# Performance work log

Hardware: AMD Instinct MI355X
Metric: run time of the kernel (lower is better)

Reference implementation:

```python
import jax, jax.numpy as jnp
import numpy as np

DIM = 1024
N_HEADS = 16
HEAD_DIM = DIM // N_HEADS  # 64
THETA = 10000.0
B, S = 4, 1024


def _rope_full_dim(x):
    """RoPE applied over the FULL last dim (head_dim == model dim), matching the
    original module which builds RotaryEmbeddings(head_dim=args.dim) and applies
    it to [B, S, dim] before splitting into heads. Positions start at 0."""
    Bx, Sx, D = x.shape
    freq = 1.0 / (THETA ** (jnp.arange(0, D, 2, dtype=jnp.float32) / D))  # [D/2]
    ang = jnp.arange(Sx, dtype=jnp.float32)[:, None] * freq[None, :]      # [S, D/2]
    cos, sin = jnp.cos(ang), jnp.sin(ang)
    xp = x.astype(jnp.float32).reshape(Bx, Sx, D // 2, 2)
    x0, x1 = xp[..., 0], xp[..., 1]
    rot = jnp.stack([x0 * cos - x1 * sin, x0 * sin + x1 * cos], axis=-1)
    return rot.reshape(Bx, Sx, D).astype(x.dtype)


def setup_inputs() -> dict:
    key = jax.random.key(0)
    ks = jax.random.split(key, 5)
    scale = 1.0 / np.sqrt(DIM)
    x = jax.random.normal(ks[0], (B, S, DIM), dtype=jnp.float32)
    Wq = jax.random.normal(ks[1], (DIM, DIM), dtype=jnp.float32) * scale
    Wk = jax.random.normal(ks[2], (DIM, DIM), dtype=jnp.float32) * scale
    Wv = jax.random.normal(ks[3], (DIM, DIM), dtype=jnp.float32) * scale
    Wo = jax.random.normal(ks[4], (DIM, DIM), dtype=jnp.float32) * scale
    bo = jnp.zeros((DIM,), dtype=jnp.float32)
    return {"x": x, "Wq": Wq, "Wk": Wk, "Wv": Wv, "Wo": Wo, "bo": bo, "start_pos": 0}


def reference(x, Wq, Wk, Wv, Wo, bo, start_pos):
    # start_pos == 0: the zero-initialized KV cache write+read is an identity
    # (keys == xk, values == xv over [:, :S]); n_rep == 1 so repeat_kv is a no-op.
    # NOTE: the original applies NO causal mask.
    Bx, Sx, _ = x.shape
    xq = _rope_full_dim(x @ Wq.T)  # [B, S, DIM] (weights stored torch-style [out,in])
    xk = _rope_full_dim(x @ Wk.T)
    xv = x @ Wv.T
    q = xq.reshape(Bx, Sx, N_HEADS, HEAD_DIM).transpose(0, 2, 1, 3)  # [B,H,S,D]
    k = xk.reshape(Bx, Sx, N_HEADS, HEAD_DIM).transpose(0, 2, 1, 3)
    v = xv.reshape(Bx, Sx, N_HEADS, HEAD_DIM).transpose(0, 2, 1, 3)
    scores = jnp.einsum("bhqd,bhkd->bhqk", q, k) / np.float32(np.sqrt(HEAD_DIM))
    attn = jax.nn.softmax(scores.astype(jnp.float32), axis=-1).astype(q.dtype)
    out = jnp.einsum("bhqk,bhkd->bhqd", attn, v)          # [B,H,S,D]
    out = out.transpose(0, 2, 1, 3).reshape(Bx, Sx, DIM)  # [B,S,DIM]
    return out @ Wo.T + bo
```

## Files before the change

### kernel.cpp

```cpp
#include <hip/hip_runtime.h>
#include <cstdint>
#include <cstddef>

typedef _Float16 f16;
typedef __attribute__((ext_vector_type(8))) _Float16 h8v;
typedef __attribute__((ext_vector_type(4))) _Float16 h4v;
typedef __attribute__((ext_vector_type(4))) float f4v;

#define DIM 1024
#define SEQ 1024
#define NH 16
#define HD 64

__device__ __forceinline__ void gld16(const void* g, void* l) {
  __builtin_amdgcn_global_load_lds(
      (const __attribute__((address_space(1))) void*)g,
      (__attribute__((address_space(3))) void*)l, 16, 0, 0);
}

__device__ __forceinline__ f4v mfma16(h8v a, h8v b, f4v c) {
  return __builtin_amdgcn_mfma_f32_16x16x32_f16(a, b, c, 0, 0, 0);
}
__device__ __forceinline__ f4v mfma16k16(h4v a, h4v b, f4v c) {
  return __builtin_amdgcn_mfma_f32_16x16x16f16(a, b, c, 0, 0, 0);
}

__device__ __forceinline__ void cvt_store4(f16* dst, float4 v) {
  *(h4v*)dst = (h4v){(f16)v.x, (f16)v.y, (f16)v.z, (f16)v.w};
}

__global__ __launch_bounds__(256) void convert_kernel(
    const float* __restrict__ x,  const float* __restrict__ Wq,
    const float* __restrict__ Wk, const float* __restrict__ Wv,
    const float* __restrict__ Wo,
    f16* __restrict__ xh, f16* __restrict__ wqkv, f16* __restrict__ woh)
{
  int i = blockIdx.x * 256 + threadIdx.x;
  cvt_store4(xh + 4 * (size_t)i, ((const float4*)x)[i]);
  if (i < DIM * DIM / 4) {
    cvt_store4(wqkv + 4 * (size_t)i,               ((const float4*)Wq)[i]);
    cvt_store4(wqkv + DIM * DIM + 4 * (size_t)i,   ((const float4*)Wk)[i]);
    cvt_store4(wqkv + 2 * DIM * DIM + 4 * (size_t)i, ((const float4*)Wv)[i]);
    cvt_store4(woh + 4 * (size_t)i,                ((const float4*)Wo)[i]);
  }
}

__global__ __launch_bounds__(256) void qkv_gemm(
    const f16* __restrict__ A, const f16* __restrict__ W,
    f16* __restrict__ Qh, f16* __restrict__ Kh, f16* __restrict__ Vt)
{
  __shared__ f16 lA[128 * 32];
  __shared__ f16 lB[128 * 32];
  const int m0 = blockIdx.x * 128;
  const int n0 = blockIdx.y * 128;
  const int tid = threadIdx.x;
  const int w = tid >> 6, lane = tid & 63, quad = lane >> 4, l16 = lane & 15;
  const int wm = (w >> 1) * 64, wn = (w & 1) * 64;

  const int c0 = tid, c1 = 256 + tid;
  const int r0 = c0 >> 2, kc0 = (c0 & 3) ^ ((r0 >> 1) & 3);
  const int r1 = c1 >> 2, kc1 = (c1 & 3) ^ ((r1 >> 1) & 3);
  const f16* gA0 = A + (size_t)(m0 + r0) * DIM + kc0 * 8;
  const f16* gA1 = A + (size_t)(m0 + r1) * DIM + kc1 * 8;
  const f16* gB0 = W + (size_t)(n0 + r0) * DIM + kc0 * 8;
  const f16* gB1 = W + (size_t)(n0 + r1) * DIM + kc1 * 8;
  f16* lA0 = &lA[(c0 & ~63) * 8];
  f16* lA1 = &lA[(c1 & ~63) * 8];
  f16* lB0 = &lB[(c0 & ~63) * 8];
  f16* lB1 = &lB[(c1 & ~63) * 8];

  int pA[4], pB[4];
#pragma unroll
  for (int t = 0; t < 4; ++t) {
    int r = wm + t * 16 + l16;
    pA[t] = r * 4 + (quad ^ ((r >> 1) & 3));
    int rn = wn + t * 16 + l16;
    pB[t] = rn * 4 + (quad ^ ((rn >> 1) & 3));
  }

  f4v acc[4][4] = {};
  for (int kt = 0; kt < DIM / 32; ++kt) {
    const int ko = kt * 32;
    gld16(gA0 + ko, lA0);
    gld16(gA1 + ko, lA1);
    gld16(gB0 + ko, lB0);
    gld16(gB1 + ko, lB1);
    __syncthreads();
    h8v af[4], bf[4];
#pragma unroll
    for (int t = 0; t < 4; ++t) af[t] = *(const h8v*)&lA[pA[t] * 8];
#pragma unroll
    for (int t = 0; t < 4; ++t) bf[t] = *(const h8v*)&lB[pB[t] * 8];
#pragma unroll
    for (int i = 0; i < 4; ++i)
#pragma unroll
      for (int j = 0; j < 4; ++j)
        acc[i][j] = mfma16(af[i], bf[j], acc[i][j]);
    __syncthreads();
  }

  if (n0 < 2 * DIM) {
    f16* dst = (n0 < DIM) ? Qh : Kh;
    const float osc = (n0 < DIM) ? 0.18033688f : 1.0f;
#pragma unroll
    for (int i = 0; i < 4; ++i) {
      const int mb = m0 + wm + i * 16 + quad * 4;
#pragma unroll
      for (int j = 0; j < 4; ++j) {
        const int n = n0 + wn + j * 16 + l16;
        const int d = n & (DIM - 1);
        const float fr = exp2f(-0.025952563f * (float)(d >> 1));
        const float sgn = (d & 1) ? 1.0f : -1.0f;
        const int hh = d >> 6, dd = d & 63;
#pragma unroll
        for (int r = 0; r < 4; ++r) {
          const int m = mb + r;
          const int s = m & (SEQ - 1), b = m >> 10;
          const float v = acc[i][j][r];
          const float pt = __shfl_xor(v, 1, 64);
          float sn, cs;
          __sincosf((float)s * fr, &sn, &cs);
          dst[((size_t)(b * NH + hh) * SEQ + s) * HD + dd] =
              (f16)((v * cs + sgn * pt * sn) * osc);
        }
      }
    }
  } else {
#pragma unroll
    for (int i = 0; i < 4; ++i) {
      const int mb = m0 + wm + i * 16 + quad * 4;
      const int s = mb & (SEQ - 1), b = mb >> 10;
#pragma unroll
      for (int j = 0; j < 4; ++j) {
        const int d = (n0 - 2 * DIM) + wn + j * 16 + l16;
        const int hh = d >> 6, dd = d & 63;
        h4v vv = {(f16)acc[i][j][0], (f16)acc[i][j][1],
                  (f16)acc[i][j][2], (f16)acc[i][j][3]};
        *(h4v*)&Vt[((size_t)(b * NH + hh) * HD + dd) * SEQ + s] = vv;
      }
    }
  }
}

__global__ __launch_bounds__(256) void attn_kernel(
    const f16* __restrict__ Q, const f16* __restrict__ K,
    const f16* __restrict__ V, f16* __restrict__ O)
{
  __shared__ f16 LK[2][4096];
  __shared__ f16 LV[2][4096];
  const int tid = threadIdx.x;
  const int w = tid >> 6, lane = tid & 63, quad = lane >> 4, l16 = lane & 15;
  const int bid = blockIdx.x;
  const int qt = bid >> 6, bh = bid & 63;
  const f16* Qb = Q + (size_t)bh * SEQ * HD;
  const f16* Kg = K + (size_t)bh * SEQ * HD;
  const f16* Vg = V + (size_t)bh * HD * SEQ;
  const int q0 = qt * 64;
  const int qrow = q0 + w * 16 + l16;

  const h8v bq0 = *(const h8v*)&Qb[(size_t)qrow * HD + quad * 8];
  const h8v bq1 = *(const h8v*)&Qb[(size_t)qrow * HD + quad * 8 + 32];

  const int c0 = tid, c1 = 256 + tid;
  const int r0 = c0 >> 3, kc0 = (c0 & 7) ^ (r0 & 7);
  const int r1 = c1 >> 3, kc1 = (c1 & 7) ^ (r1 & 7);
  const f16* gK0 = Kg + (size_t)r0 * HD + kc0 * 8;
  const f16* gK1 = Kg + (size_t)r1 * HD + kc1 * 8;
  const f16* gV0 = Vg + (size_t)r0 * SEQ + kc0 * 8;
  const f16* gV1 = Vg + (size_t)r1 * SEQ + kc1 * 8;
  const int dk0 = (c0 & ~63) * 8, dk1 = (c1 & ~63) * 8;

  int koff[4][2];
#pragma unroll
  for (int j = 0; j < 4; ++j) {
    int r = j * 16 + l16;
#pragma unroll
    for (int kk = 0; kk < 2; ++kk)
      koff[j][kk] = (r * 8 + ((quad + 4 * kk) ^ (r & 7))) * 8;
  }
  int voff[4];
#pragma unroll
  for (int j = 0; j < 4; ++j) {
    int slot = (j * 2 + (quad >> 1)) ^ (l16 & 7);
    voff[j] = l16 * 64 + slot * 8 + (quad & 1) * 4;
  }

  float lr = 0.f;
  f4v accO[4] = {};

#define ATTN_PREF(TT, BUF)                       \
  {                                              \
    const size_t kb = (size_t)(TT) * 64;         \
    gld16(gK0 + kb * HD, &LK[BUF][dk0]);         \
    gld16(gK1 + kb * HD, &LK[BUF][dk1]);         \
    gld16(gV0 + kb, &LV[BUF][dk0]);              \
    gld16(gV1 + kb, &LV[BUF][dk1]);              \
  }

#define ATTN_TILE(BUF)                                                       \
  {                                                                          \
    f4v sc[4];                                                               \
    _Pragma("unroll")                                                        \
    for (int j = 0; j < 4; ++j) {                                            \
      f4v z = {-12.f, -12.f, -12.f, -12.f};           \
      z = mfma16(*(const h8v*)&LK[BUF][koff[j][0]], bq0, z);                 \
      z = mfma16(*(const h8v*)&LK[BUF][koff[j][1]], bq1, z);                 \
      sc[j] = z;                                                             \
    }                                                                        \
    float rs = 0.f;                                                          \
    h4v pf[4];                                                               \
    _Pragma("unroll")                                                        \
    for (int j = 0; j < 4; ++j) {                                            \
      float p0 = exp2f(sc[j][0]), p1 = exp2f(sc[j][1]);                      \
      float p2 = exp2f(sc[j][2]), p3 = exp2f(sc[j][3]);                      \
      rs += (p0 + p1) + (p2 + p3);                                           \
      pf[j] = (h4v){(f16)p0, (f16)p1, (f16)p2, (f16)p3};                     \
    }                                                                        \
    rs += __shfl_xor(rs, 16, 64);                                            \
    rs += __shfl_xor(rs, 32, 64);                                            \
    lr += rs;                                                                \
    _Pragma("unroll")                                                        \
    for (int dt = 0; dt < 4; ++dt)                                           \
      _Pragma("unroll")                                                      \
      for (int j = 0; j < 4; ++j)                                            \
        accO[dt] = mfma16k16(pf[j], *(const h4v*)&LV[BUF][voff[j] + dt * 1024], \
                             accO[dt]);                                      \
  }

  ATTN_PREF(0, 0);
  for (int t = 0; t < SEQ / 64; t += 2) {
    __syncthreads();
    ATTN_PREF(t + 1, 1);
    ATTN_TILE(0);
    __syncthreads();
    if (t + 2 < SEQ / 64) ATTN_PREF(t + 2, 0);
    ATTN_TILE(1);
  }
#undef ATTN_PREF
#undef ATTN_TILE

  f4v invl;
#pragma unroll
  for (int r = 0; r < 4; ++r) invl[r] = 1.0f / __shfl(lr, quad * 4 + r, 64);

  const int b = bh >> 4, hh = bh & 15;
#pragma unroll
  for (int dt = 0; dt < 4; ++dt) {
    const int d = dt * 16 + l16;
#pragma unroll
    for (int r = 0; r < 4; ++r) {
      const int s = q0 + w * 16 + quad * 4 + r;
      O[(size_t)(b * SEQ + s) * DIM + hh * HD + d] = (f16)(accO[dt][r] * invl[r]);
    }
  }
}

__global__ __launch_bounds__(256) void out_gemm(
    const f16* __restrict__ A, const f16* __restrict__ W,
    const float* __restrict__ bias, float* __restrict__ out)
{
  __shared__ f16 lA[64 * 32];
  __shared__ f16 lB[128 * 32];
  const int m0 = blockIdx.x * 64;
  const int n0 = blockIdx.y * 128;
  const int tid = threadIdx.x;
  const int w = tid >> 6, lane = tid & 63, quad = lane >> 4, l16 = lane & 15;
  const int wm = (w >> 1) * 32, wn = (w & 1) * 64;

  const int c0 = tid, c1 = 256 + tid;
  const int rA = c0 >> 2, kcA = (c0 & 3) ^ ((rA >> 1) & 3);
  const int rB1 = c1 >> 2, kcB1 = (c1 & 3) ^ ((rB1 >> 1) & 3);
  const f16* gA  = A + (size_t)(m0 + rA) * DIM + kcA * 8;
  const f16* gB0 = W + (size_t)(n0 + rA) * DIM + kcA * 8;
  const f16* gB1 = W + (size_t)(n0 + rB1) * DIM + kcB1 * 8;
  f16* lAp  = &lA[(c0 & ~63) * 8];
  f16* lB0p = &lB[(c0 & ~63) * 8];
  f16* lB1p = &lB[(c1 & ~63) * 8];

  int pA_[2], pB_[4];
#pragma unroll
  for (int t = 0; t < 2; ++t) {
    int r = wm + t * 16 + l16;
    pA_[t] = r * 4 + (quad ^ ((r >> 1) & 3));
  }
#pragma unroll
  for (int t = 0; t < 4; ++t) {
    int rn = wn + t * 16 + l16;
    pB_[t] = rn * 4 + (quad ^ ((rn >> 1) & 3));
  }

  f4v acc[2][4] = {};
  for (int kt = 0; kt < DIM / 32; ++kt) {
    const int ko = kt * 32;
    gld16(gA + ko, lAp);
    gld16(gB0 + ko, lB0p);
    gld16(gB1 + ko, lB1p);
    __syncthreads();
    h8v af[2], bf[4];
#pragma unroll
    for (int t = 0; t < 2; ++t) af[t] = *(const h8v*)&lA[pA_[t] * 8];
#pragma unroll
    for (int t = 0; t < 4; ++t) bf[t] = *(const h8v*)&lB[pB_[t] * 8];
#pragma unroll
    for (int i = 0; i < 2; ++i)
#pragma unroll
      for (int j = 0; j < 4; ++j)
        acc[i][j] = mfma16(af[i], bf[j], acc[i][j]);
    __syncthreads();
  }

#pragma unroll
  for (int i = 0; i < 2; ++i) {
#pragma unroll
    for (int j = 0; j < 4; ++j) {
      const int n = n0 + wn + j * 16 + l16;
      const float bv = bias[n];
#pragma unroll
      for (int r = 0; r < 4; ++r) {
        const int m = m0 + wm + i * 16 + quad * 4 + r;
        out[(size_t)m * DIM + n] = acc[i][j][r] + bv;
      }
    }
  }
}

extern "C" void kernel_launch(void* const* d_in, const int* in_sizes, int n_in,
                              void* d_out, int out_size, void* d_ws, size_t ws_size,
                              hipStream_t stream)
{
  (void)in_sizes; (void)n_in; (void)out_size; (void)ws_size;
  const float* x  = (const float*)d_in[0];
  const float* Wq = (const float*)d_in[1];
  const float* Wk = (const float*)d_in[2];
  const float* Wv = (const float*)d_in[3];
  const float* Wo = (const float*)d_in[4];
  const float* bo = (const float*)d_in[5];
  float* out = (float*)d_out;

  char* ws = (char*)d_ws;
  const size_t MB = (size_t)1 << 20;
  f16* xh   = (f16*)(ws);
  f16* wqkv = (f16*)(ws + 8  * MB);
  f16* woh  = (f16*)(ws + 14 * MB);
  f16* Qh   = (f16*)(ws + 16 * MB);
  f16* Kh   = (f16*)(ws + 24 * MB);
  f16* Vt   = (f16*)(ws + 32 * MB);
  f16* Oh   = (f16*)(ws);

  convert_kernel<<<dim3(4096), 256, 0, stream>>>(x, Wq, Wk, Wv, Wo, xh, wqkv, woh);
  qkv_gemm<<<dim3(32, 24), 256, 0, stream>>>(xh, wqkv, Qh, Kh, Vt);
  attn_kernel<<<dim3(1024), 256, 0, stream>>>(Qh, Kh, Vt, Oh);
  out_gemm<<<dim3(64, 8), 256, 0, stream>>>(Oh, woh, bo, out);
}
```

Baseline: 181.5 us.

## Process two query tiles per attention block and compute row sums via MFMA

Each attention block now handles 128 query rows instead of 64, so each wave reuses every K and V fragment loaded from LDS for two query sub-tiles and the grid halves. The softmax row-sum is computed with an extra MFMA against a ones vector on fp16-summed probabilities instead of a float reduction with cross-lane shuffles. This cuts K/V global and LDS traffic per query but doubles accumulator registers, which may lower occupancy, and summing probabilities in fp16 loses some precision.

```diff
diff --git a/kernel.cpp b/kernel.cpp
--- a/kernel.cpp
+++ b/kernel.cpp
@@ -155,11 +155,12 @@
   const f16* Qb = Q + (size_t)bh * SEQ * HD;
   const f16* Kg = K + (size_t)bh * SEQ * HD;
   const f16* Vg = V + (size_t)bh * HD * SEQ;
-  const int q0 = qt * 64;
-  const int qrow = q0 + w * 16 + l16;
-
-  const h8v bq0 = *(const h8v*)&Qb[(size_t)qrow * HD + quad * 8];
-  const h8v bq1 = *(const h8v*)&Qb[(size_t)qrow * HD + quad * 8 + 32];
+  const int q0 = qt * 128 + w * 16;
+
+  const h8v bq0a = *(const h8v*)&Qb[(size_t)(q0 + l16) * HD + quad * 8];
+  const h8v bq0b = *(const h8v*)&Qb[(size_t)(q0 + l16) * HD + quad * 8 + 32];
+  const h8v bq1a = *(const h8v*)&Qb[(size_t)(q0 + 64 + l16) * HD + quad * 8];
+  const h8v bq1b = *(const h8v*)&Qb[(size_t)(q0 + 64 + l16) * HD + quad * 8 + 32];
 
   const int c0 = tid, c1 = 256 + tid;
   const int r0 = c0 >> 3, kc0 = (c0 & 7) ^ (r0 & 7);
@@ -185,8 +186,9 @@
     voff[j] = l16 * 64 + slot * 8 + (quad & 1) * 4;
   }
 
-  float lr = 0.f;
-  f4v accO[4] = {};
+  const h4v vones = {(f16)1.f, (f16)1.f, (f16)1.f, (f16)1.f};
+  f4v accL0 = {}, accL1 = {};
+  f4v accO0[4] = {}, accO1[4] = {};
 
 #define ATTN_PREF(TT, BUF)                       \
   {                                              \
@@ -199,32 +201,45 @@
 
 #define ATTN_TILE(BUF)                                                       \
   {                                                                          \
-    f4v sc[4];                                                               \
+    h8v kf[4][2];                                                            \
     _Pragma("unroll")                                                        \
     for (int j = 0; j < 4; ++j) {                                            \
-      f4v z = {-12.f, -12.f, -12.f, -12.f};           \
-      z = mfma16(*(const h8v*)&LK[BUF][koff[j][0]], bq0, z);                 \
-      z = mfma16(*(const h8v*)&LK[BUF][koff[j][1]], bq1, z);                 \
-      sc[j] = z;                                                             \
+      kf[j][0] = *(const h8v*)&LK[BUF][koff[j][0]];                          \
+      kf[j][1] = *(const h8v*)&LK[BUF][koff[j][1]];                          \
     }                                                                        \
-    float rs = 0.f;                                                          \
-    h4v pf[4];                                                               \
+    f4v sc0[4], sc1[4];                                                      \
     _Pragma("unroll")                                                        \
     for (int j = 0; j < 4; ++j) {                                            \
-      float p0 = exp2f(sc[j][0]), p1 = exp2f(sc[j][1]);                      \
-      float p2 = exp2f(sc[j][2]), p3 = exp2f(sc[j][3]);                      \
-      rs += (p0 + p1) + (p2 + p3);                                           \
-      pf[j] = (h4v){(f16)p0, (f16)p1, (f16)p2, (f16)p3};                     \
+      f4v z0 = {-12.f, -12.f, -12.f, -12.f};          \
+      z0 = mfma16(kf[j][0], bq0a, z0);                                       \
+      z0 = mfma16(kf[j][1], bq0b, z0);                                       \
+      sc0[j] = z0;                                                           \
+      f4v z1 = {-12.f, -12.f, -12.f, -12.f};                                 \
+      z1 = mfma16(kf[j][0], bq1a, z1);                                       \
+      z1 = mfma16(kf[j][1], bq1b, z1);                                       \
+      sc1[j] = z1;                                                           \
     }                                                                        \
-    rs += __shfl_xor(rs, 16, 64);                                            \
-    rs += __shfl_xor(rs, 32, 64);                                            \
-    lr += rs;                                                                \
+    h4v pf0[4], pf1[4];                                                      \
     _Pragma("unroll")                                                        \
-    for (int dt = 0; dt < 4; ++dt)                                           \
+    for (int j = 0; j < 4; ++j) {                                            \
+      pf0[j] = (h4v){(f16)exp2f(sc0[j][0]), (f16)exp2f(sc0[j][1]),           \
+                     (f16)exp2f(sc0[j][2]), (f16)exp2f(sc0[j][3])};          \
+      pf1[j] = (h4v){(f16)exp2f(sc1[j][0]), (f16)exp2f(sc1[j][1]),           \
+                     (f16)exp2f(sc1[j][2]), (f16)exp2f(sc1[j][3])};          \
+    }                                                                        \
+    h4v ps0 = (pf0[0] + pf0[1]) + (pf0[2] + pf0[3]);                         \
+    h4v ps1 = (pf1[0] + pf1[1]) + (pf1[2] + pf1[3]);                         \
+    accL0 = mfma16k16(ps0, vones, accL0);                                    \
+    accL1 = mfma16k16(ps1, vones, accL1);                                    \
+    _Pragma("unroll")                                                        \
+    for (int dt = 0; dt < 4; ++dt) {                                         \
       _Pragma("unroll")                                                      \
-      for (int j = 0; j < 4; ++j)                                            \
-        accO[dt] = mfma16k16(pf[j], *(const h4v*)&LV[BUF][voff[j] + dt * 1024], \
-                             accO[dt]);                                      \
+      for (int j = 0; j < 4; ++j) {                                          \
+        const h4v vf = *(const h4v*)&LV[BUF][voff[j] + dt * 1024];           \
+        accO0[dt] = mfma16k16(pf0[j], vf, accO0[dt]);                        \
+        accO1[dt] = mfma16k16(pf1[j], vf, accO1[dt]);                        \
+      }                                                                      \
+    }                                                                        \
   }
 
   ATTN_PREF(0, 0);
@@ -239,18 +254,17 @@
 #undef ATTN_PREF
 #undef ATTN_TILE
 
-  f4v invl;
-#pragma unroll
-  for (int r = 0; r < 4; ++r) invl[r] = 1.0f / __shfl(lr, quad * 4 + r, 64);
-
   const int b = bh >> 4, hh = bh & 15;
 #pragma unroll
   for (int dt = 0; dt < 4; ++dt) {
     const int d = dt * 16 + l16;
 #pragma unroll
     for (int r = 0; r < 4; ++r) {
-      const int s = q0 + w * 16 + quad * 4 + r;
-      O[(size_t)(b * SEQ + s) * DIM + hh * HD + d] = (f16)(accO[dt][r] * invl[r]);
+      const int s0 = q0 + quad * 4 + r;
+      O[(size_t)(b * SEQ + s0) * DIM + hh * HD + d] =
+          (f16)(accO0[dt][r] / accL0[r]);
+      O[(size_t)(b * SEQ + s0 + 64) * DIM + hh * HD + d] =
+          (f16)(accO1[dt][r] / accL1[r]);
     }
   }
 }
@@ -349,6 +363,6 @@
 
   convert_kernel<<<dim3(4096), 256, 0, stream>>>(x, Wq, Wk, Wv, Wo, xh, wqkv, woh);
   qkv_gemm<<<dim3(32, 24), 256, 0, stream>>>(xh, wqkv, Qh, Kh, Vt);
-  attn_kernel<<<dim3(1024), 256, 0, stream>>>(Qh, Kh, Vt, Oh);
+  attn_kernel<<<dim3(512), 256, 0, stream>>>(Qh, Kh, Vt, Oh);
   out_gemm<<<dim3(64, 8), 256, 0, stream>>>(Oh, woh, bo, out);
 }
```

After: 173.8 us. 4.2% less time.
